# Performance work log

Measured on AMD Instinct MI355X. Metric: run time of the kernel, lower is better.

Reference implementation:

```python
import jax, jax.numpy as jnp
import numpy as np
import math

B, L, IN_DIM = 2, 2048, 32
D_MODEL, NHEAD, D_FF, N_LAYERS, NUM_CLASSES = 256, 8, 1024, 2, 8
FACTOR = 5
D_K = D_MODEL // NHEAD
U = min(L, int(FACTOR * math.log(L)))  # ProbSparse top-k size = 38
LN_EPS = 1e-5


def setup_inputs() -> dict:
    key = jax.random.key(0)
    ks = jax.random.split(key, 16)
    s = 0.02
    d = {
        "x": jax.random.normal(ks[0], (B, L, IN_DIM), jnp.float32),
        "emb_w": jax.random.normal(ks[1], (IN_DIM, D_MODEL), jnp.float32) * s,
        "emb_b": jnp.zeros((D_MODEL,), jnp.float32),
        "wq": jax.random.normal(ks[2], (N_LAYERS, D_MODEL, D_MODEL), jnp.float32) * s,
        "bq": jnp.zeros((N_LAYERS, D_MODEL), jnp.float32),
        "wk": jax.random.normal(ks[3], (N_LAYERS, D_MODEL, D_MODEL), jnp.float32) * s,
        "bk": jnp.zeros((N_LAYERS, D_MODEL), jnp.float32),
        "wv": jax.random.normal(ks[4], (N_LAYERS, D_MODEL, D_MODEL), jnp.float32) * s,
        "bv": jnp.zeros((N_LAYERS, D_MODEL), jnp.float32),
        "wo": jax.random.normal(ks[5], (N_LAYERS, D_MODEL, D_MODEL), jnp.float32) * s,
        "bo": jnp.zeros((N_LAYERS, D_MODEL), jnp.float32),
        "ln1_g": jnp.ones((N_LAYERS, D_MODEL), jnp.float32),
        "ln1_b": jnp.zeros((N_LAYERS, D_MODEL), jnp.float32),
        "ln2_g": jnp.ones((N_LAYERS, D_MODEL), jnp.float32),
        "ln2_b": jnp.zeros((N_LAYERS, D_MODEL), jnp.float32),
        "ff1_w": jax.random.normal(ks[6], (N_LAYERS, D_MODEL, D_FF), jnp.float32) * s,
        "ff1_b": jnp.zeros((N_LAYERS, D_FF), jnp.float32),
        "ff2_w": jax.random.normal(ks[7], (N_LAYERS, D_FF, D_MODEL), jnp.float32) * s,
        "ff2_b": jnp.zeros((N_LAYERS, D_MODEL), jnp.float32),
        "dec_w": jax.random.normal(ks[8], (D_MODEL, NUM_CLASSES), jnp.float32) * s,
        "dec_b": jnp.zeros((NUM_CLASSES,), jnp.float32),
    }
    return d


def _pos_encoding(L, d):
    pos = jnp.arange(L, dtype=jnp.float32)[:, None]              # [L,1]
    div = jnp.exp(jnp.arange(0, d, 2, dtype=jnp.float32) * (-math.log(10000.0) / d))
    sin, cos = jnp.sin(pos * div), jnp.cos(pos * div)            # [L,d/2]
    return jnp.stack([sin, cos], axis=-1).reshape(L, d)          # interleave sin/cos


def _layernorm(h, g, b):
    m = jnp.mean(h, axis=-1, keepdims=True)
    v = jnp.mean((h - m) ** 2, axis=-1, keepdims=True)
    return (h - m) * jax.lax.rsqrt(v + LN_EPS) * g + b


def _prob_sparse_attn(h, wq, bq, wk, bk, wv, bv, wo, bo):
    Bb, Ll, _ = h.shape
    q = (h @ wq + bq).reshape(Bb, Ll, NHEAD, D_K).transpose(0, 2, 1, 3)  # [B,H,L,D]
    k = (h @ wk + bk).reshape(Bb, Ll, NHEAD, D_K).transpose(0, 2, 1, 3)
    v = (h @ wv + bv).reshape(Bb, Ll, NHEAD, D_K).transpose(0, 2, 1, 3)
    scores = jnp.einsum('bhld,bhmd->bhlm', q, k) / math.sqrt(D_K)        # [B,H,L,L]
    thr = jax.lax.top_k(scores, U)[0][..., -1:]                          # U-th largest per row
    scores = jnp.where(scores >= thr, scores, -jnp.inf)
    attn = jax.nn.softmax(scores, axis=-1)
    ctx = jnp.einsum('bhlm,bhmd->bhld', attn, v)
    ctx = ctx.transpose(0, 2, 1, 3).reshape(Bb, Ll, D_MODEL)
    return ctx @ wo + bo


def reference(x, emb_w, emb_b, wq, bq, wk, bk, wv, bv, wo, bo,
              ln1_g, ln1_b, ln2_g, ln2_b, ff1_w, ff1_b, ff2_w, ff2_b,
              dec_w, dec_b):
    h = (x @ emb_w + emb_b) * math.sqrt(D_MODEL)
    h = h + _pos_encoding(h.shape[1], D_MODEL)[None]
    for l in range(N_LAYERS):
        a = _prob_sparse_attn(h, wq[l], bq[l], wk[l], bk[l], wv[l], bv[l], wo[l], bo[l])
        h = _layernorm(h + a, ln1_g[l], ln1_b[l])
        ff = jax.nn.relu(h @ ff1_w[l] + ff1_b[l]) @ ff2_w[l] + ff2_b[l]
        h = _layernorm(h + ff, ln2_g[l], ln2_b[l])
    return h @ dec_w + dec_b
```

## Files before the change

kernel.cpp:

```cpp
#include <hip/hip_runtime.h>
#include <math.h>

#define D_MODEL 256
#define NHEAD   8
#define D_K     32
#define LSEQ    2048
#define BATCH   2
#define ROWS    (BATCH * LSEQ)
#define D_FF    1024
#define UTOP    38
#define CAP     128

__global__ __launch_bounds__(256) void k_embed(const float* __restrict__ x,
                                               const float* __restrict__ w,
                                               const float* __restrict__ b,
                                               float* __restrict__ h) {
    int row = blockIdx.x;
    int l   = row & (LSEQ - 1);
    int d   = threadIdx.x;
    __shared__ float xs[32];
    if (d < 32) xs[d] = x[row * 32 + d];
    __syncthreads();
    float acc = 0.f;
#pragma unroll
    for (int i = 0; i < 32; ++i) acc += xs[i] * w[i * D_MODEL + d];
    acc = (acc + b[d]) * 16.0f;
    int m = d >> 1;
    float div = expf(-(float)(2 * m) * (9.210340371976184f / 256.0f));
    float ang = (float)l * div;
    float pe = (d & 1) ? cosf(ang) : sinf(ang);
    h[row * D_MODEL + d] = acc + pe;
}

template <int MODE>
__device__ __forceinline__ void gemm_body(const float* __restrict__ A, int lda,
                                          const float* __restrict__ W, int N,
                                          const float* __restrict__ bias, bool doBias,
                                          float* __restrict__ C, int K,
                                          int m0, int n0) {
    __shared__ float As[16][68];
    __shared__ float Ws[16][68];
    const int t  = threadIdx.x;
    const int tx = t & 15, ty = t >> 4;
    float acc[4][4] = {};
    for (int k0 = 0; k0 < K; k0 += 16) {
        {
            int mr = t >> 2, kc = (t & 3) * 4;
            float4 av = *(const float4*)&A[(size_t)(m0 + mr) * lda + k0 + kc];
            As[kc + 0][mr] = av.x; As[kc + 1][mr] = av.y;
            As[kc + 2][mr] = av.z; As[kc + 3][mr] = av.w;
            int kr = t >> 4, nc = (t & 15) * 4;
            *(float4*)&Ws[kr][nc] = *(const float4*)&W[(size_t)(k0 + kr) * N + n0 + nc];
        }
        __syncthreads();
#pragma unroll
        for (int k = 0; k < 16; ++k) {
            float4 a4 = *(const float4*)&As[k][ty * 4];
            float4 w4 = *(const float4*)&Ws[k][tx * 4];
            float av[4] = {a4.x, a4.y, a4.z, a4.w};
            float wv[4] = {w4.x, w4.y, w4.z, w4.w};
#pragma unroll
            for (int i = 0; i < 4; ++i)
#pragma unroll
                for (int j = 0; j < 4; ++j) acc[i][j] += av[i] * wv[j];
        }
        __syncthreads();
    }
#pragma unroll
    for (int i = 0; i < 4; ++i) {
        int row = m0 + ty * 4 + i;
#pragma unroll
        for (int j = 0; j < 4; ++j) {
            int col = n0 + tx * 4 + j;
            float v = acc[i][j];
            if (doBias) v += bias[col];
            if (MODE == 1) v = fmaxf(v, 0.f);
            if (MODE == 2) {
                int bb = row >> 11, ll = row & (LSEQ - 1);
                int hh = col >> 5, dd = col & 31;
                C[(((size_t)(bb * NHEAD + hh) * LSEQ) + ll) * D_K + dd] = v;
            } else {
                C[(size_t)row * N + col] = v;
            }
        }
    }
}

__global__ __launch_bounds__(256) void k_qkv(const float* __restrict__ A,
                                             const float* __restrict__ wq,
                                             const float* __restrict__ wk,
                                             const float* __restrict__ wv,
                                             const float* __restrict__ bq,
                                             const float* __restrict__ bk,
                                             const float* __restrict__ bv,
                                             float* __restrict__ out) {
    int z = blockIdx.z;
    const float* W = z == 0 ? wq : (z == 1 ? wk : wv);
    const float* B = z == 0 ? bq : (z == 1 ? bk : bv);
    gemm_body<2>(A, 256, W, 256, B, true, out + (size_t)z * (1 << 20), 256,
                 blockIdx.x * 64, blockIdx.y * 64);
}

__global__ __launch_bounds__(256) void k_gemm_sk(const float* __restrict__ A, int lda,
                                                 const float* __restrict__ W,
                                                 const float* __restrict__ bias,
                                                 float* __restrict__ Cbase,
                                                 int N, int Ksub) {
    int z = blockIdx.z;
    gemm_body<0>(A + (size_t)z * Ksub, lda, W + (size_t)z * Ksub * N, N, bias, z == 0,
                 Cbase + (size_t)z * (1 << 20), Ksub, blockIdx.x * 64, blockIdx.y * 64);
}

__global__ __launch_bounds__(256) void k_ff1(const float* __restrict__ A,
                                             const float* __restrict__ W,
                                             const float* __restrict__ bias,
                                             float* __restrict__ C) {
    gemm_body<1>(A, 256, W, 1024, bias, true, C, 256, blockIdx.x * 64, blockIdx.y * 64);
}

__device__ __forceinline__ unsigned int sortkey(float f) {
    unsigned int u = __float_as_uint(f);
    return (u & 0x80000000u) ? ~u : (u | 0x80000000u);
}
__device__ __forceinline__ float key2f(unsigned int u) {
    unsigned int b = (u & 0x80000000u) ? (u ^ 0x80000000u) : ~u;
    return __uint_as_float(b);
}
__device__ __forceinline__ void gload_lds16(const float* src, float* ldsDst) {
    __builtin_amdgcn_global_load_lds(
        (const __attribute__((address_space(1))) unsigned int*)src,
        (__attribute__((address_space(3))) unsigned int*)ldsDst,
        16, 0, 0);
}

__global__ __launch_bounds__(256, 3) void k_attn(const float* __restrict__ Q,
                                                 const float* __restrict__ Kt,
                                                 const float* __restrict__ Vt,
                                                 float* __restrict__ ctxb) {
    __shared__ float          Kl[3][2048];
    __shared__ unsigned int   lvk[4][2][CAP];
    __shared__ unsigned short lix[4][2][CAP];
    __shared__ int            bins[4][16];
    __shared__ int            lcnt[4][2];

    const int tid   = threadIdx.x;
    const int lane  = tid & 63;
    const int wid   = tid >> 6;
    const int lbid  = (blockIdx.x & 7) * 512 + (blockIdx.x >> 3);
    const int bh    = lbid >> 8;
    const int chunk = lbid & 255;
    const int row0  = chunk * 8 + wid * 2;
    const int b     = bh >> 3, hh = bh & 7;

    const float* Kb = Kt + (size_t)bh * LSEQ * D_K;
    const float* Vb = Vt + (size_t)bh * LSEQ * D_K;
    const float* qp = Q + ((size_t)bh * LSEQ + row0) * D_K;

    const float scale = 0.17677669529663687f;
    float q0[32], q1[32];
#pragma unroll
    for (int i = 0; i < 32; ++i) {
        q0[i] = qp[i] * scale;
        q1[i] = qp[32 + i] * scale;
    }

#define STAGE(T, SLOT)                                                          \
    {                                                                           \
        int g0_ = wid * 2, g1_ = wid * 2 + 1;                                   \
        gload_lds16(Kb + (size_t)(T) * 2048 + lane * 32 + g0_ * 4,              \
                    &Kl[SLOT][g0_ * 256]);                                      \
        gload_lds16(Kb + (size_t)(T) * 2048 + lane * 32 + g1_ * 4,              \
                    &Kl[SLOT][g1_ * 256]);                                      \
    }

    unsigned int k0[32], k1[32];
    unsigned int lm0 = 0u, lm1 = 0u;

    STAGE(0, 0)
    STAGE(1, 1)
    asm volatile("s_waitcnt vmcnt(2)" ::: "memory");
    __builtin_amdgcn_s_barrier();

#pragma unroll
    for (int t = 0; t < 32; ++t) {
        const int slot = t % 3;
        if (t < 30) STAGE(t + 2, (t + 2) % 3)
        float a0 = 0.f, a1 = 0.f;
#pragma unroll
        for (int u = 0; u < 8; ++u) {
            float4 kv = *(const float4*)&Kl[slot][u * 256 + lane * 4];
            a0 += q0[u*4+0]*kv.x + q0[u*4+1]*kv.y + q0[u*4+2]*kv.z + q0[u*4+3]*kv.w;
            a1 += q1[u*4+0]*kv.x + q1[u*4+1]*kv.y + q1[u*4+2]*kv.z + q1[u*4+3]*kv.w;
        }
        k0[t] = sortkey(a0);
        k1[t] = sortkey(a1);
        if (k0[t] > lm0) lm0 = k0[t];
        if (k1[t] > lm1) lm1 = k1[t];
        if (t < 31) {
            if (t < 30) asm volatile("s_waitcnt vmcnt(2)" ::: "memory");
            else        asm volatile("s_waitcnt vmcnt(0)" ::: "memory");
            __builtin_amdgcn_s_barrier();
        }
    }

    unsigned int Tpiv[2];
    float        rmaxf[2];
#pragma unroll
    for (int r = 0; r < 2; ++r) {
        unsigned int v = r ? lm1 : lm0;
#pragma unroll
        for (int k = 2; k <= 64; k <<= 1) {
#pragma unroll
            for (int j = k >> 1; j >= 1; j >>= 1) {
                unsigned int pv = (unsigned int)__shfl_xor((int)v, j);
                bool lower = ((lane & j) == 0);
                bool up    = ((lane & k) == 0);
                unsigned int mn = v < pv ? v : pv;
                unsigned int mx = v < pv ? pv : v;
                v = (lower == up) ? mn : mx;
            }
        }
        Tpiv[r]  = (unsigned int)__shfl((int)v, 26);
        rmaxf[r] = key2f((unsigned int)__shfl((int)v, 63));
    }
    if (lane < 2) lcnt[wid][lane] = 0;

#pragma unroll
    for (int j = 0; j < 32; ++j) {
        if (k0[j] >= Tpiv[0]) {
            int s = atomicAdd(&lcnt[wid][0], 1);
            if (s < CAP) { lvk[wid][0][s] = k0[j]; lix[wid][0][s] = (unsigned short)(j * 64 + lane); }
        }
        if (k1[j] >= Tpiv[1]) {
            int s = atomicAdd(&lcnt[wid][1], 1);
            if (s < CAP) { lvk[wid][1][s] = k1[j]; lix[wid][1][s] = (unsigned short)(j * 64 + lane); }
        }
    }

    const int h = lane >> 5;
    const int p = lane & 31;
#pragma unroll
    for (int r = 0; r < 2; ++r) {
        int cnt = lcnt[wid][r]; if (cnt > CAP) cnt = CAP;

        unsigned int prefix = 0;
        int need = UTOP;
#pragma unroll
        for (int pass = 0; pass < 8; ++pass) {
            const int sh = 28 - pass * 4;
            if (lane < 16) bins[wid][lane] = 0;
            for (int i = lane; i < cnt; i += 64) {
                unsigned int key = lvk[wid][r][i];
                bool msk = (pass == 0) || ((key >> (sh + 4)) == (prefix >> (sh + 4)));
                if (msk) atomicAdd(&bins[wid][(key >> sh) & 15], 1);
            }
            int c = (lane < 16) ? bins[wid][lane] : 0;
            int suf = c;
#pragma unroll
            for (int off = 1; off < 16; off <<= 1) {
                int o = __shfl_down(suf, off);
                suf += (lane + off < 16) ? o : 0;
            }
            int above = suf - c;
            bool found = (lane < 16) && (above < need) && (above + c >= need);
            unsigned int cp = prefix | ((unsigned int)lane << sh);
            int cn = need - above;
            unsigned long long bal = __ballot(found);
            int wl = (int)(__ffsll(bal) - 1);
            prefix = (unsigned int)__shfl((int)cp, wl);
            need   = __shfl(cn, wl);
        }
        const unsigned int thrkey = prefix;

        float psum = 0.f;
        for (int i = lane; i < cnt; i += 64) {
            unsigned int key = lvk[wid][r][i];
            if (key >= thrkey) psum += expf(key2f(key) - rmaxf[r]);
        }
#pragma unroll
        for (int off = 32; off >= 1; off >>= 1) psum += __shfl_xor(psum, off);
        float inv = 1.0f / psum;

        float acc = 0.f;
        for (int i = h; i < cnt; i += 2) {
            unsigned int key = lvk[wid][r][i];
            float w = (key >= thrkey) ? expf(key2f(key) - rmaxf[r]) : 0.f;
            acc += w * Vb[(size_t)lix[wid][r][i] * D_K + p];
        }
        acc += __shfl_xor(acc, 32);
        if (lane < 32)
            ctxb[((size_t)(b * LSEQ) + row0 + r) * D_MODEL + hh * D_K + p] = acc * inv;
    }
}

__global__ __launch_bounds__(64) void k_addln2(float* __restrict__ h,
                                               const float* __restrict__ a1,
                                               const float* __restrict__ a2,
                                               const float* __restrict__ g,
                                               const float* __restrict__ bb) {
    int row = blockIdx.x, lane = threadIdx.x;
    float4 hv = *(const float4*)&h[(size_t)row * D_MODEL + lane * 4];
    float4 v1 = *(const float4*)&a1[(size_t)row * D_MODEL + lane * 4];
    float4 v2 = *(const float4*)&a2[(size_t)row * D_MODEL + lane * 4];
    float x0 = hv.x + v1.x + v2.x, x1 = hv.y + v1.y + v2.y;
    float x2 = hv.z + v1.z + v2.z, x3 = hv.w + v1.w + v2.w;
    float s = x0 + x1 + x2 + x3;
#pragma unroll
    for (int off = 32; off >= 1; off >>= 1) s += __shfl_xor(s, off);
    float mean = s * (1.0f / 256.0f);
    float d0 = x0 - mean, d1 = x1 - mean, d2 = x2 - mean, d3 = x3 - mean;
    float vs = d0 * d0 + d1 * d1 + d2 * d2 + d3 * d3;
#pragma unroll
    for (int off = 32; off >= 1; off >>= 1) vs += __shfl_xor(vs, off);
    float inv = rsqrtf(vs * (1.0f / 256.0f) + 1e-5f);
    float4 gv = *(const float4*)&g[lane * 4];
    float4 bv = *(const float4*)&bb[lane * 4];
    float4 o;
    o.x = d0 * inv * gv.x + bv.x;
    o.y = d1 * inv * gv.y + bv.y;
    o.z = d2 * inv * gv.z + bv.z;
    o.w = d3 * inv * gv.w + bv.w;
    *(float4*)&h[(size_t)row * D_MODEL + lane * 4] = o;
}

__global__ __launch_bounds__(64) void k_dec(const float* __restrict__ h,
                                            const float* __restrict__ w,
                                            const float* __restrict__ b,
                                            float* __restrict__ out) {
    int row = blockIdx.x, lane = threadIdx.x;
    int c = lane & 7, part = lane >> 3;
    float acc = 0.f;
    int d0 = part * 32;
#pragma unroll
    for (int dd = 0; dd < 32; ++dd) acc += h[(size_t)row * D_MODEL + d0 + dd] * w[(d0 + dd) * 8 + c];
    acc += __shfl_xor(acc, 8);
    acc += __shfl_xor(acc, 16);
    acc += __shfl_xor(acc, 32);
    if (lane < 8) out[(size_t)row * 8 + c] = acc + b[c];
}

extern "C" void kernel_launch(void* const* d_in, const int* in_sizes, int n_in,
                              void* d_out, int out_size, void* d_ws, size_t ws_size,
                              hipStream_t stream) {
    const float* x     = (const float*)d_in[0];
    const float* emb_w = (const float*)d_in[1];
    const float* emb_b = (const float*)d_in[2];
    const float* wq    = (const float*)d_in[3];
    const float* bq    = (const float*)d_in[4];
    const float* wk    = (const float*)d_in[5];
    const float* bk    = (const float*)d_in[6];
    const float* wv    = (const float*)d_in[7];
    const float* bv    = (const float*)d_in[8];
    const float* wo    = (const float*)d_in[9];
    const float* bo    = (const float*)d_in[10];
    const float* ln1_g = (const float*)d_in[11];
    const float* ln1_b = (const float*)d_in[12];
    const float* ln2_g = (const float*)d_in[13];
    const float* ln2_b = (const float*)d_in[14];
    const float* ff1_w = (const float*)d_in[15];
    const float* ff1_b = (const float*)d_in[16];
    const float* ff2_w = (const float*)d_in[17];
    const float* ff2_b = (const float*)d_in[18];
    const float* dec_w = (const float*)d_in[19];
    const float* dec_b = (const float*)d_in[20];

    float* ws   = (float*)d_ws;
    float* h    = ws;
    float* qb   = h    + (1 << 20);
    float* kb   = qb   + (1 << 20);
    float* vb   = kb   + (1 << 20);
    float* ctxb = vb   + (1 << 20);
    float* ffb  = ctxb + (1 << 20);

    k_embed<<<ROWS, 256, 0, stream>>>(x, emb_w, emb_b, h);

    for (int l = 0; l < 2; ++l) {
        const float* wql = wq + (size_t)l * 65536;  const float* bql = bq + l * 256;
        const float* wkl = wk + (size_t)l * 65536;  const float* bkl = bk + l * 256;
        const float* wvl = wv + (size_t)l * 65536;  const float* bvl = bv + l * 256;
        const float* wol = wo + (size_t)l * 65536;  const float* bol = bo + l * 256;

        dim3 gq(64, 4, 3);
        k_qkv<<<gq, 256, 0, stream>>>(h, wql, wkl, wvl, bql, bkl, bvl, qb);

        k_attn<<<NHEAD * BATCH * 256, 256, 0, stream>>>(qb, kb, vb, ctxb);

        dim3 gsk(64, 4, 2);
        k_gemm_sk<<<gsk, 256, 0, stream>>>(ctxb, 256, wol, bol, qb, 256, 128);
        k_addln2<<<ROWS, 64, 0, stream>>>(h, qb, kb, ln1_g + l * 256, ln1_b + l * 256);

        dim3 gf1(64, 16);
        k_ff1<<<gf1, 256, 0, stream>>>(h, ff1_w + (size_t)l * 262144, ff1_b + l * 1024, ffb);

        k_gemm_sk<<<gsk, 256, 0, stream>>>(ffb, 1024, ff2_w + (size_t)l * 262144,
                                           ff2_b + l * 256, qb, 256, 512);
        k_addln2<<<ROWS, 64, 0, stream>>>(h, qb, kb, ln2_g + l * 256, ln2_b + l * 256);
    }

    k_dec<<<ROWS, 64, 0, stream>>>(h, dec_w, dec_b, (float*)d_out);
}
```

Measured before the change: 868.1 us.

## Split head dim across half-waves for QK and use bitonic sort for top-k threshold

The QK score loop now has each half-wave hold 16 of the 32 query dimensions, and partial dot products are combined with a cross-half shuffle. This halves the query registers and changes the K staging layout so each lane handles two keys. The 8-pass radix-histogram threshold search, with its LDS atomics, is replaced by a 128-element bitonic sort in registers across two values per lane. The sort adds more shuffles but removes LDS atomics and the bins array, and the interleaved key indexing has to map correctly back to V rows.

```diff
diff --git a/kernel.cpp b/kernel.cpp
--- a/kernel.cpp
+++ b/kernel.cpp
@@ -140,7 +140,6 @@
     __shared__ float          Kl[3][2048];
     __shared__ unsigned int   lvk[4][2][CAP];
     __shared__ unsigned short lix[4][2][CAP];
-    __shared__ int            bins[4][16];
     __shared__ int            lcnt[4][2];
 
     const int tid   = threadIdx.x;
@@ -151,26 +150,28 @@
     const int chunk = lbid & 255;
     const int row0  = chunk * 8 + wid * 2;
     const int b     = bh >> 3, hh = bh & 7;
+    const int h     = lane >> 5;
+    const int p     = lane & 31;
 
     const float* Kb = Kt + (size_t)bh * LSEQ * D_K;
     const float* Vb = Vt + (size_t)bh * LSEQ * D_K;
     const float* qp = Q + ((size_t)bh * LSEQ + row0) * D_K;
 
     const float scale = 0.17677669529663687f;
-    float q0[32], q1[32];
-#pragma unroll
-    for (int i = 0; i < 32; ++i) {
-        q0[i] = qp[i] * scale;
-        q1[i] = qp[32 + i] * scale;
+    float q0[16], q1[16];
+#pragma unroll
+    for (int i = 0; i < 16; ++i) {
+        q0[i] = qp[h * 16 + i] * scale;
+        q1[i] = qp[32 + h * 16 + i] * scale;
     }
 
 #define STAGE(T, SLOT)                                                          \
     {                                                                           \
-        int g0_ = wid * 2, g1_ = wid * 2 + 1;                                   \
-        gload_lds16(Kb + (size_t)(T) * 2048 + lane * 32 + g0_ * 4,              \
-                    &Kl[SLOT][g0_ * 256]);                                      \
-        gload_lds16(Kb + (size_t)(T) * 2048 + lane * 32 + g1_ * 4,              \
-                    &Kl[SLOT][g1_ * 256]);                                      \
+        const int g0_ = wid * 2, g1_ = wid * 2 + 1;                             \
+        gload_lds16(Kb + (size_t)(T) * 2048 + (2 * p + (g0_ >> 2)) * 32         \
+                        + h * 16 + (g0_ & 3) * 4, &Kl[SLOT][g0_ * 256]);        \
+        gload_lds16(Kb + (size_t)(T) * 2048 + (2 * p + (g1_ >> 2)) * 32         \
+                        + h * 16 + (g1_ & 3) * 4, &Kl[SLOT][g1_ * 256]);        \
     }
 
     unsigned int k0[32], k1[32];
@@ -185,15 +186,22 @@
     for (int t = 0; t < 32; ++t) {
         const int slot = t % 3;
         if (t < 30) STAGE(t + 2, (t + 2) % 3)
-        float a0 = 0.f, a1 = 0.f;
-#pragma unroll
-        for (int u = 0; u < 8; ++u) {
-            float4 kv = *(const float4*)&Kl[slot][u * 256 + lane * 4];
-            a0 += q0[u*4+0]*kv.x + q0[u*4+1]*kv.y + q0[u*4+2]*kv.z + q0[u*4+3]*kv.w;
-            a1 += q1[u*4+0]*kv.x + q1[u*4+1]*kv.y + q1[u*4+2]*kv.z + q1[u*4+3]*kv.w;
-        }
-        k0[t] = sortkey(a0);
-        k1[t] = sortkey(a1);
+        float a0 = 0.f, a1 = 0.f, e0 = 0.f, e1 = 0.f;
+#pragma unroll
+        for (int c = 0; c < 4; ++c) {
+            float4 kva = *(const float4*)&Kl[slot][c * 256 + lane * 4];
+            float4 kvb = *(const float4*)&Kl[slot][(4 + c) * 256 + lane * 4];
+            a0 += q0[c*4+0]*kva.x + q0[c*4+1]*kva.y + q0[c*4+2]*kva.z + q0[c*4+3]*kva.w;
+            a1 += q1[c*4+0]*kva.x + q1[c*4+1]*kva.y + q1[c*4+2]*kva.z + q1[c*4+3]*kva.w;
+            e0 += q0[c*4+0]*kvb.x + q0[c*4+1]*kvb.y + q0[c*4+2]*kvb.z + q0[c*4+3]*kvb.w;
+            e1 += q1[c*4+0]*kvb.x + q1[c*4+1]*kvb.y + q1[c*4+2]*kvb.z + q1[c*4+3]*kvb.w;
+        }
+        float fA0 = a0 + __shfl_xor(a0, 32);
+        float fB0 = e0 + __shfl_xor(e0, 32);
+        float fA1 = a1 + __shfl_xor(a1, 32);
+        float fB1 = e1 + __shfl_xor(e1, 32);
+        k0[t] = sortkey(h ? fB0 : fA0);
+        k1[t] = sortkey(h ? fB1 : fA1);
         if (k0[t] > lm0) lm0 = k0[t];
         if (k1[t] > lm1) lm1 = k1[t];
         if (t < 31) {
@@ -229,48 +237,42 @@
     for (int j = 0; j < 32; ++j) {
         if (k0[j] >= Tpiv[0]) {
             int s = atomicAdd(&lcnt[wid][0], 1);
-            if (s < CAP) { lvk[wid][0][s] = k0[j]; lix[wid][0][s] = (unsigned short)(j * 64 + lane); }
+            if (s < CAP) { lvk[wid][0][s] = k0[j]; lix[wid][0][s] = (unsigned short)(j * 64 + 2 * p + h); }
         }
         if (k1[j] >= Tpiv[1]) {
             int s = atomicAdd(&lcnt[wid][1], 1);
-            if (s < CAP) { lvk[wid][1][s] = k1[j]; lix[wid][1][s] = (unsigned short)(j * 64 + lane); }
-        }
-    }
-
-    const int h = lane >> 5;
-    const int p = lane & 31;
+            if (s < CAP) { lvk[wid][1][s] = k1[j]; lix[wid][1][s] = (unsigned short)(j * 64 + 2 * p + h); }
+        }
+    }
+
 #pragma unroll
     for (int r = 0; r < 2; ++r) {
         int cnt = lcnt[wid][r]; if (cnt > CAP) cnt = CAP;
 
-        unsigned int prefix = 0;
-        int need = UTOP;
-#pragma unroll
-        for (int pass = 0; pass < 8; ++pass) {
-            const int sh = 28 - pass * 4;
-            if (lane < 16) bins[wid][lane] = 0;
-            for (int i = lane; i < cnt; i += 64) {
-                unsigned int key = lvk[wid][r][i];
-                bool msk = (pass == 0) || ((key >> (sh + 4)) == (prefix >> (sh + 4)));
-                if (msk) atomicAdd(&bins[wid][(key >> sh) & 15], 1);
+        unsigned int v0 = (lane < cnt)      ? lvk[wid][r][lane]      : 0u;
+        unsigned int v1 = (64 + lane < cnt) ? lvk[wid][r][64 + lane] : 0u;
+#pragma unroll
+        for (int k = 2; k <= 128; k <<= 1) {
+#pragma unroll
+            for (int j = k >> 1; j >= 1; j >>= 1) {
+                if (j >= 64) {
+                    bool up0 = ((lane & k) == 0);
+                    unsigned int mn = v0 < v1 ? v0 : v1;
+                    unsigned int mx = v0 < v1 ? v1 : v0;
+                    v0 = up0 ? mn : mx;
+                    v1 = up0 ? mx : mn;
+                } else {
+                    unsigned int p0 = (unsigned int)__shfl_xor((int)v0, j);
+                    unsigned int p1 = (unsigned int)__shfl_xor((int)v1, j);
+                    bool lower = ((lane & j) == 0);
+                    bool up0 = (((lane) & k) == 0);
+                    bool up1 = (((64 + lane) & k) == 0);
+                    v0 = (lower == up0) ? (v0 < p0 ? v0 : p0) : (v0 < p0 ? p0 : v0);
+                    v1 = (lower == up1) ? (v1 < p1 ? v1 : p1) : (v1 < p1 ? p1 : v1);
+                }
             }
-            int c = (lane < 16) ? bins[wid][lane] : 0;
-            int suf = c;
-#pragma unroll
-            for (int off = 1; off < 16; off <<= 1) {
-                int o = __shfl_down(suf, off);
-                suf += (lane + off < 16) ? o : 0;
-            }
-            int above = suf - c;
-            bool found = (lane < 16) && (above < need) && (above + c >= need);
-            unsigned int cp = prefix | ((unsigned int)lane << sh);
-            int cn = need - above;
-            unsigned long long bal = __ballot(found);
-            int wl = (int)(__ffsll(bal) - 1);
-            prefix = (unsigned int)__shfl((int)cp, wl);
-            need   = __shfl(cn, wl);
-        }
-        const unsigned int thrkey = prefix;
+        }
+        const unsigned int thrkey = (unsigned int)__shfl((int)v1, 26);
 
         float psum = 0.f;
         for (int i = lane; i < cnt; i += 64) {
```

New measurement: 831.0 us. 4.3% less time.
